# Kernel tuning notes

Measured on AMD Instinct MI355X. Metric: run time of the kernel, lower is better.

The kernel has to match this reference:

```python
import jax, jax.numpy as jnp
import numpy as np

B, S, D, H, F, E = 2, 1024, 1024, 16, 2048, 8
HD = D // H


def _ln(x, g, b, eps=1e-5):
    m = x.mean(-1, keepdims=True)
    v = ((x - m) ** 2).mean(-1, keepdims=True)
    return (x - m) / jnp.sqrt(v + eps) * g + b


def setup_inputs() -> dict:
    key = jax.random.key(0)
    ks = jax.random.split(key, 12)
    rn = lambda k, shp, s=0.02: jax.random.normal(k, shp, jnp.float32) * s
    return {
        'src': jax.random.normal(ks[0], (B, S, D), jnp.float32),
        'q_w': rn(ks[1], (D, D)),
        'k_w': rn(ks[2], (D, D)),
        'v_w': rn(ks[3], (D, D)),
        'out_w': rn(ks[4], (D, D)),
        'gate_w': rn(ks[5], (D, D)),
        'gate_b': rn(ks[6], (D,)),
        'scale_w': rn(ks[7], (H, HD)),
        'n1_g': jnp.ones((D,), jnp.float32),
        'n1_b': jnp.zeros((D,), jnp.float32),
        'n2_g': jnp.ones((D,), jnp.float32),
        'n2_b': jnp.zeros((D,), jnp.float32),
        'moe_gate_w': rn(ks[8], (D, E)),
        'moe_gate_b': jnp.zeros((E,), jnp.float32),
        'w1': rn(ks[9], (E, D, F)),
        'b1': jnp.zeros((E, F), jnp.float32),
        'ln_g': jnp.ones((E, F), jnp.float32),
        'ln_b': jnp.zeros((E, F), jnp.float32),
        'w2': rn(ks[10], (E, F, D)),
        'b2': jnp.zeros((E, D), jnp.float32),
        'res_scale': jnp.ones((E,), jnp.float32),
    }


def reference(src, q_w, k_w, v_w, out_w, gate_w, gate_b, scale_w,
              n1_g, n1_b, n2_g, n2_b, moe_gate_w, moe_gate_b,
              w1, b1, ln_g, ln_b, w2, b2, res_scale):
    b, s, d = src.shape
    h = scale_w.shape[0]
    hd = d // h
    # --- MemoAttention (gated, dynamically scaled), eval mode ---
    q = (src @ q_w).reshape(b, s, h, hd).transpose(0, 2, 1, 3)  # [b,h,s,hd]
    k = (src @ k_w).reshape(b, s, h, hd).transpose(0, 2, 1, 3)
    v = (src @ v_w).reshape(b, s, h, hd).transpose(0, 2, 1, 3)
    scores = jnp.einsum('bhqd,bhkd->bhqk', q, k) / np.float32(np.sqrt(hd))
    scale = jax.nn.sigmoid(jnp.einsum('bhsd,hd->bhs', q, scale_w)) * 2.0
    scores = scores * scale[..., None]
    aw = jax.nn.softmax(scores, axis=-1)
    out = jnp.einsum('bhqk,bhkd->bhqd', aw, v).transpose(0, 2, 1, 3).reshape(b, s, d)
    gate = jax.nn.sigmoid(out @ gate_w + gate_b)
    attn = (out * gate) @ out_w
    # --- residual + norm1 ---
    x = _ln(src + attn, n1_g, n1_b)
    # --- MoE FFN (top-2 routing; torch loop overwrites -> last (max-index) expert
    xr = x.reshape(-1, d)                      # [N, d]
    n = xr.shape[0]
    logits = xr @ moe_gate_w + moe_gate_b       # [N, E]
    top_v, top_i = jax.lax.top_k(logits, 2)
    wts = jax.nn.softmax(top_v, axis=-1)        # [N, 2]
    chosen = jnp.max(top_i, axis=-1)            # last-written expert per token

    def expert(W1, B1, G, Bt, W2, B2, rsc):
        hh = xr @ W1 + B1                       # [N, F]
        hh = jax.nn.gelu(_ln(hh, G, Bt), approximate=False)
        return (hh @ W2 + B2) * rsc + xr        # [N, d]

    outs = jax.vmap(expert)(w1, b1, ln_g, ln_b, w2, b2, res_scale)  # [E,N,d]
    sel = jnp.take_along_axis(outs.transpose(1, 0, 2), chosen[:, None, None], axis=1)[:, 0]
    moe = sel * jnp.sum(wts, axis=-1, keepdims=True)
    # --- residual + norm2 ---
    return _ln(x + moe.reshape(b, s, d), n2_g, n2_b)
```

## Files before the change

kernel.cpp:

```cpp
#include <hip/hip_runtime.h>


typedef _Float16 f16;
typedef _Float16 f16x8 __attribute__((ext_vector_type(8)));
typedef _Float16 f16x4 __attribute__((ext_vector_type(4)));
typedef float f32x4 __attribute__((ext_vector_type(4)));

constexpr int CS  = 1024;
constexpr int CD  = 1024;
constexpr int CH  = 16;
constexpr int CHD = 64;
constexpr int CF  = 2048;
constexpr int CE  = 8;
constexpr int CN  = 2048;
constexpr int CBH = 32;
constexpr int KS  = 512;
constexpr int MAXT = 24;

constexpr float LO_SCALE = 2048.f;
constexpr float LO_INV   = 1.f / 2048.f;

#define MFMA16(a, b, c) __builtin_amdgcn_mfma_f32_16x16x32_f16((a), (b), (c), 0, 0, 0)

#define TO_GBL(p) ((const __attribute__((address_space(1))) void*)(p))
#define TO_LDS(p) ((__attribute__((address_space(3))) void*)(p))
#define GLD16(g, l) __builtin_amdgcn_global_load_lds(TO_GBL(g), TO_LDS(l), 16, 0, 0)

__device__ __forceinline__ void fsplit(float v, f16 &hi, f16 &lo) {
  hi = (f16)v;
  lo = (f16)((v - (float)hi) * LO_SCALE);
}


__global__ void k_split_cvt(const float* __restrict__ in, f16* __restrict__ oh,
                            f16* __restrict__ ol, int n) {
  int i = (blockIdx.x * blockDim.x + threadIdx.x) * 4;
  if (i >= n) return;
  float4 v = *(const float4*)(in + i);
  float a[4] = {v.x, v.y, v.z, v.w};
  f16x4 vh, vl;
#pragma unroll
  for (int j = 0; j < 4; ++j) {
    f16 hi = (f16)a[j];
    vh[j] = hi;
    vl[j] = (f16)((a[j] - (float)hi) * LO_SCALE);
  }
  *(f16x4*)(oh + i) = vh;
  *(f16x4*)(ol + i) = vl;
}

__global__ __launch_bounds__(256) void k_transpose_split(
    const float* __restrict__ in, f16* __restrict__ oh,
    f16* __restrict__ ol, int R, int C) {
  __shared__ float t[64][65];
  const int z = blockIdx.z;
  const float* src = in + (size_t)z * R * C;
  f16* dh = oh + (size_t)z * R * C;
  f16* dl = ol ? ol + (size_t)z * R * C : nullptr;
  const int c0 = blockIdx.x * 64, r0 = blockIdx.y * 64;
  const int tt = threadIdx.x;
  const int lane = tt & 63, wv = tt >> 6;
#pragma unroll
  for (int i = 0; i < 16; ++i)
    t[wv + i * 4][lane] = src[(size_t)(r0 + wv + i * 4) * C + c0 + lane];
  __syncthreads();
  const int oc = tt >> 4;
  const int og = tt & 15;
#pragma unroll
  for (int cc = 0; cc < 64; cc += 16) {
    f16x4 vh, vl;
#pragma unroll
    for (int j = 0; j < 4; ++j) {
      const float v = t[og * 4 + j][cc + oc];
      f16 hi = (f16)v;
      vh[j] = hi;
      vl[j] = (f16)((v - (float)hi) * LO_SCALE);
    }
    const size_t idx = (size_t)(c0 + cc + oc) * R + r0 + og * 4;
    *(f16x4*)(dh + idx) = vh;
    if (dl) *(f16x4*)(dl + idx) = vl;
  }
}


template <bool SPLIT>
__device__ __forceinline__ void gemm_tile128(
    const f16* a0, const f16* a1, const f16* al0, const f16* al1,
    const f16* b0, const f16* b1, const f16* bl0, const f16* bl1,
    int K, f16* lds, f32x4 (&accm)[4][4], f32x4 (&accc)[4][4]) {
  constexpr int BUF = SPLIT ? 16384 : 8192;
  constexpr int BO  = SPLIT ? 8192 : 4096;
  const int t = threadIdx.x;
  const int lane = t & 63, wave = t >> 6;
  const int wm = wave >> 1, wn = wave & 1;
  const int m16 = lane & 15, quad = lane >> 4;
  int aoff[4], boff[4];
#pragma unroll
  for (int s = 0; s < 4; ++s) {
    const int ra = wm * 64 + s * 16 + m16;
    aoff[s] = ra * 32 + ((quad ^ ((ra >> 1) & 3)) * 8);
    const int rb = wn * 64 + s * 16 + m16;
    boff[s] = BO + rb * 32 + ((quad ^ ((rb >> 1) & 3)) * 8);
  }
  auto stage = [&](f16* buf) {
    GLD16(a0, buf + t * 8);
    GLD16(a1, buf + 2048 + t * 8);
    GLD16(b0, buf + BO + t * 8);
    GLD16(b1, buf + BO + 2048 + t * 8);
    if constexpr (SPLIT) {
      GLD16(al0, buf + 4096 + t * 8);
      GLD16(al1, buf + 6144 + t * 8);
      GLD16(bl0, buf + 12288 + t * 8);
      GLD16(bl1, buf + 14336 + t * 8);
      al0 += 32; al1 += 32; bl0 += 32; bl1 += 32;
    }
    a0 += 32; a1 += 32; b0 += 32; b1 += 32;
  };
  stage(lds);
  int cur = 0;
  for (int k = 0; k < K; k += 32) {
    __syncthreads();
    f16* buf = lds + cur * BUF;
    if (k + 32 < K) stage(lds + (cur ^ 1) * BUF);
    f16x8 af[4], alf[4];
#pragma unroll
    for (int s = 0; s < 4; ++s) {
      af[s] = *(const f16x8*)(buf + aoff[s]);
      if constexpr (SPLIT) alf[s] = *(const f16x8*)(buf + 4096 + aoff[s]);
    }
#pragma unroll
    for (int sn = 0; sn < 4; ++sn) {
      const f16x8 bf = *(const f16x8*)(buf + boff[sn]);
#pragma unroll
      for (int sm = 0; sm < 4; ++sm)
        accm[sm][sn] = MFMA16(af[sm], bf, accm[sm][sn]);
      if constexpr (SPLIT) {
        const f16x8 blf = *(const f16x8*)(buf + 4096 + boff[sn]);
#pragma unroll
        for (int sm = 0; sm < 4; ++sm)
          accc[sm][sn] = MFMA16(af[sm], blf, accc[sm][sn]);
#pragma unroll
        for (int sm = 0; sm < 4; ++sm)
          accc[sm][sn] = MFMA16(alf[sm], bf, accc[sm][sn]);
      }
    }
    cur ^= 1;
  }
}


__global__ __launch_bounds__(256, 2) void g_qkv(
    const f16* __restrict__ srcH, const f16* __restrict__ srcL,
    const f16* __restrict__ qwH, const f16* __restrict__ qwL,
    const f16* __restrict__ kwH, const f16* __restrict__ kwL,
    const f16* __restrict__ vwH, const f16* __restrict__ vwL,
    f16* __restrict__ qHo, f16* __restrict__ qLo,
    f16* __restrict__ kHo, f16* __restrict__ kLo,
    f16* __restrict__ vTH, f16* __restrict__ vTL) {
  __shared__ f16 lds[32768];
  const int z = blockIdx.z;
  const int m0 = blockIdx.x * 128, n0 = blockIdx.y * 128;
  const int t = threadIdx.x;
  const int rowS = t >> 2;
  const int ksw = ((t & 3) ^ ((rowS >> 1) & 3)) * 8;
  const f16* BH = (z == 0) ? qwH : (z == 1) ? kwH : vwH;
  const f16* BL = (z == 0) ? qwL : (z == 1) ? kwL : vwL;
  const f16* A0 = srcH + (size_t)(m0 + rowS) * CD + ksw;
  const f16* AL0 = srcL + (size_t)(m0 + rowS) * CD + ksw;
  const f16* B0 = BH + (size_t)(n0 + rowS) * CD + ksw;
  const f16* BL0 = BL + (size_t)(n0 + rowS) * CD + ksw;
  const f32x4 VZ = {0.f, 0.f, 0.f, 0.f};
  f32x4 accm[4][4], accc[4][4];
#pragma unroll
  for (int i = 0; i < 4; ++i)
#pragma unroll
    for (int j = 0; j < 4; ++j) { accm[i][j] = VZ; accc[i][j] = VZ; }
  gemm_tile128<true>(A0, A0 + (size_t)64 * CD, AL0, AL0 + (size_t)64 * CD,
                     B0, B0 + (size_t)64 * CD, BL0, BL0 + (size_t)64 * CD,
                     CD, lds, accm, accc);
  const int lane = t & 63, wave = t >> 6;
  const int wm = wave >> 1, wn = wave & 1;
  const int m16 = lane & 15, quad = lane >> 4;
#pragma unroll
  for (int sm = 0; sm < 4; ++sm)
#pragma unroll
    for (int sn = 0; sn < 4; ++sn)
#pragma unroll
      for (int r = 0; r < 4; ++r) {
        const int row = m0 + wm * 64 + sm * 16 + quad * 4 + r;
        const int col = n0 + wn * 64 + sn * 16 + m16;
        const float v = accm[sm][sn][r] + accc[sm][sn][r] * LO_INV;
        f16 hi, lo; fsplit(v, hi, lo);
        const int bb = row >> 10, ss = row & 1023;
        const int hh = col >> 6, hd = col & 63;
        if (z == 2) {
          const size_t idx = ((size_t)((bb * CH + hh) * CHD + hd)) * CS + ss;
          vTH[idx] = hi; vTL[idx] = lo;
        } else {
          const size_t idx = ((size_t)((bb * CH + hh) * CS + ss)) * CHD + hd;
          if (z == 0) { qHo[idx] = hi; qLo[idx] = lo; }
          else        { kHo[idx] = hi; kLo[idx] = lo; }
        }
      }
}


__device__ __forceinline__ int pswz(int q, int k) {
  return q * 64 + ((((k >> 2) ^ q) & 15) << 2) + (k & 3);
}

__global__ __launch_bounds__(256) void k_fattn(
    const f16* __restrict__ qH_, const f16* __restrict__ qL_,
    const f16* __restrict__ kH_, const f16* __restrict__ kL_,
    const f16* __restrict__ vTH_, const f16* __restrict__ vTL_,
    const float* __restrict__ scale_w,
    f16* __restrict__ aoH, f16* __restrict__ aoL) {
  __shared__ f16 kvb[32768];
  __shared__ float psc[4 * 1024];
  const int bh = blockIdx.y;
  const int b = bh >> 4, h = bh & 15;
  const int t = threadIdx.x;
  const int lane = t & 63, wave = t >> 6;
  const int m16 = lane & 15, quad = lane >> 4;
  const int q0 = blockIdx.x * 64 + wave * 16;
  float* P = psc + wave * 1024;
  const f32x4 VZ = {0.f, 0.f, 0.f, 0.f};
  const size_t kb = (size_t)bh * CS * CHD;

  const int rowS = t >> 3, chS = t & 7;
  auto stage = [&](f16* dst, int kc) {
#pragma unroll
    for (int i = 0; i < 2; ++i) {
      const int row = rowS + 32 * i;
      const int sc = (chS ^ (row & 7)) * 8;
      GLD16(kH_ + kb + (size_t)(kc + row) * CHD + sc, dst + i * 2048 + t * 8);
      GLD16(kL_ + kb + (size_t)(kc + row) * CHD + sc, dst + 4096 + i * 2048 + t * 8);
      GLD16(vTH_ + kb + (size_t)row * CS + kc + sc, dst + 8192 + i * 2048 + t * 8);
      GLD16(vTL_ + kb + (size_t)row * CS + kc + sc, dst + 12288 + i * 2048 + t * 8);
    }
  };
  auto ldf = [&](const f16* piece, int r, int q) -> f16x8 {
    return *(const f16x8*)(piece + r * 64 + ((q ^ (r & 7)) * 8));
  };

  const f16* qrh = qH_ + ((size_t)bh * CS + q0 + m16) * CHD + quad * 8;
  const f16* qrl = qL_ + ((size_t)bh * CS + q0 + m16) * CHD + quad * 8;
  f16x8 a0h = *(const f16x8*)(qrh);
  f16x8 a1h = *(const f16x8*)(qrh + 32);
  f16x8 a0l = *(const f16x8*)(qrl);
  f16x8 a1l = *(const f16x8*)(qrl + 32);

  stage(kvb, 0);

  float dot = 0.f;
  {
    const float* sw = scale_w + h * CHD + quad * 8;
    float4 s0 = *(const float4*)(sw);
    float4 s1 = *(const float4*)(sw + 4);
    float4 s2 = *(const float4*)(sw + 32);
    float4 s3 = *(const float4*)(sw + 36);
    float sv[16] = {s0.x, s0.y, s0.z, s0.w, s1.x, s1.y, s1.z, s1.w,
                    s2.x, s2.y, s2.z, s2.w, s3.x, s3.y, s3.z, s3.w};
#pragma unroll
    for (int j = 0; j < 8; ++j) {
      dot += ((float)a0h[j] + (float)a0l[j] * LO_INV) * sv[j];
      dot += ((float)a1h[j] + (float)a1l[j] * LO_INV) * sv[8 + j];
    }
    dot += __shfl_xor(dot, 16);
    dot += __shfl_xor(dot, 32);
  }
  const float qsv = 2.f / (1.f + __expf(-dot));
  float qsr[4];
#pragma unroll
  for (int r = 0; r < 4; ++r) qsr[r] = __shfl(qsv, quad * 4 + r) * 0.125f;

  f32x4 accm[4], accc[4], accd[4];
#pragma unroll
  for (int tt = 0; tt < 4; ++tt) { accm[tt] = VZ; accc[tt] = VZ; accd[tt] = VZ; }
  float mrun[4], lrun[4];
#pragma unroll
  for (int r = 0; r < 4; ++r) { mrun[r] = -1e30f; lrun[r] = 0.f; }

  int cur = 0;
  for (int kc = 0; kc < CS; kc += 64) {
    __syncthreads();
    const f16* kv = kvb + cur * 16384;
    if (kc + 64 < CS) stage(kvb + (cur ^ 1) * 16384, kc + 64);

    f32x4 st[4];
#pragma unroll
    for (int tt = 0; tt < 4; ++tt) {
      const int r = tt * 16 + m16;
      f16x8 b0h = ldf(kv,        r, quad);
      f16x8 b1h = ldf(kv,        r, quad + 4);
      f16x8 b0l = ldf(kv + 4096, r, quad);
      f16x8 b1l = ldf(kv + 4096, r, quad + 4);
      f32x4 am = VZ, ac1 = VZ, ac2 = VZ;
      am = MFMA16(a0h, b0h, am); am = MFMA16(a1h, b1h, am);
      ac1 = MFMA16(a0h, b0l, ac1); ac2 = MFMA16(a0l, b0h, ac2);
      ac1 = MFMA16(a1h, b1l, ac1); ac2 = MFMA16(a1l, b1h, ac2);
#pragma unroll
      for (int r4 = 0; r4 < 4; ++r4)
        st[tt][r4] = (am[r4] + (ac1[r4] + ac2[r4]) * LO_INV) * qsr[r4];
    }
    float alpha[4];
#pragma unroll
    for (int r = 0; r < 4; ++r) {
      float mx = fmaxf(fmaxf(st[0][r], st[1][r]), fmaxf(st[2][r], st[3][r]));
#pragma unroll
      for (int msk = 8; msk >= 1; msk >>= 1) mx = fmaxf(mx, __shfl_xor(mx, msk));
      const float mnew = fmaxf(mrun[r], mx);
      alpha[r] = __expf(mrun[r] - mnew);
      mrun[r] = mnew;
    }
    float rs[4] = {0.f, 0.f, 0.f, 0.f};
#pragma unroll
    for (int tt = 0; tt < 4; ++tt)
#pragma unroll
      for (int r = 0; r < 4; ++r) {
        const float e = __expf(st[tt][r] - mrun[r]);
        rs[r] += e;
        P[pswz(quad * 4 + r, tt * 16 + m16)] = e;
      }
#pragma unroll
    for (int r = 0; r < 4; ++r) {
#pragma unroll
      for (int msk = 8; msk >= 1; msk >>= 1) rs[r] += __shfl_xor(rs[r], msk);
      lrun[r] = lrun[r] * alpha[r] + rs[r];
#pragma unroll
      for (int tt = 0; tt < 4; ++tt) {
        accm[tt][r] *= alpha[r]; accc[tt][r] *= alpha[r]; accd[tt][r] *= alpha[r];
      }
    }
    f16x8 pah[2], pal[2];
#pragma unroll
    for (int c = 0; c < 2; ++c) {
      const int k0 = c * 32 + quad * 8;
      float4 p0 = *(const float4*)(P + pswz(m16, k0));
      float4 p1 = *(const float4*)(P + pswz(m16, k0 + 4));
      float pv[8] = {p0.x, p0.y, p0.z, p0.w, p1.x, p1.y, p1.z, p1.w};
#pragma unroll
      for (int j = 0; j < 8; ++j) {
        f16 hi = (f16)pv[j];
        pah[c][j] = hi;
        pal[c][j] = (f16)((pv[j] - (float)hi) * LO_SCALE);
      }
    }
#pragma unroll
    for (int c = 0; c < 2; ++c)
#pragma unroll
      for (int tt = 0; tt < 4; ++tt) {
        const int r = tt * 16 + m16;
        f16x8 vbh = ldf(kv + 8192,  r, quad + 4 * c);
        f16x8 vbl = ldf(kv + 12288, r, quad + 4 * c);
        accm[tt] = MFMA16(pah[c], vbh, accm[tt]);
        accc[tt] = MFMA16(pah[c], vbl, accc[tt]);
        accd[tt] = MFMA16(pal[c], vbh, accd[tt]);
      }
    cur ^= 1;
  }
#pragma unroll
  for (int tt = 0; tt < 4; ++tt)
#pragma unroll
    for (int r = 0; r < 4; ++r) {
      const int row = q0 + quad * 4 + r;
      const float v =
          (accm[tt][r] + (accc[tt][r] + accd[tt][r]) * LO_INV) / lrun[r];
      f16 hi, lo; fsplit(v, hi, lo);
      const size_t idx = ((size_t)(b * CS + row)) * CD + h * CHD + tt * 16 + m16;
      aoH[idx] = hi; aoL[idx] = lo;
    }
}


__global__ __launch_bounds__(256, 2) void g_gate(
    const f16* __restrict__ aoH, const f16* __restrict__ aoL,
    const f16* __restrict__ gwH, const f16* __restrict__ gwL,
    float* __restrict__ gpre ) {
  __shared__ f16 lds[32768];
  const int m0 = blockIdx.x * 128, n0 = blockIdx.y * 128, s = blockIdx.z;
  const int t = threadIdx.x;
  const int rowS = t >> 2;
  const int ksw = ((t & 3) ^ ((rowS >> 1) & 3)) * 8;
  const int k0 = s * KS;
  const f16* A0 = aoH + (size_t)(m0 + rowS) * CD + k0 + ksw;
  const f16* AL0 = aoL + (size_t)(m0 + rowS) * CD + k0 + ksw;
  const f16* B0 = gwH + (size_t)(n0 + rowS) * CD + k0 + ksw;
  const f16* BL0 = gwL + (size_t)(n0 + rowS) * CD + k0 + ksw;
  const f32x4 VZ = {0.f, 0.f, 0.f, 0.f};
  f32x4 accm[4][4], accc[4][4];
#pragma unroll
  for (int i = 0; i < 4; ++i)
#pragma unroll
    for (int j = 0; j < 4; ++j) { accm[i][j] = VZ; accc[i][j] = VZ; }
  gemm_tile128<true>(A0, A0 + (size_t)64 * CD, AL0, AL0 + (size_t)64 * CD,
                     B0, B0 + (size_t)64 * CD, BL0, BL0 + (size_t)64 * CD,
                     KS, lds, accm, accc);
  float* gp = gpre + (size_t)s * CN * CD;
  const int lane = t & 63, wave = t >> 6;
  const int wm = wave >> 1, wn = wave & 1;
  const int m16 = lane & 15, quad = lane >> 4;
#pragma unroll
  for (int sm = 0; sm < 4; ++sm)
#pragma unroll
    for (int sn = 0; sn < 4; ++sn)
#pragma unroll
      for (int r = 0; r < 4; ++r) {
        const int row = m0 + wm * 64 + sm * 16 + quad * 4 + r;
        const int col = n0 + wn * 64 + sn * 16 + m16;
        gp[(size_t)row * CD + col] = accm[sm][sn][r] + accc[sm][sn][r] * LO_INV;
      }
}

__global__ __launch_bounds__(256) void k_gatemul(
    const float* __restrict__ gpre, const f16* __restrict__ aoH,
    const f16* __restrict__ aoL, const float* __restrict__ gate_b,
    f16* __restrict__ gdH, f16* __restrict__ gdL) {
  const int i = (blockIdx.x * 256 + threadIdx.x) * 4;
  float4 p0 = *(const float4*)(gpre + i);
  float4 p1 = *(const float4*)(gpre + (size_t)CN * CD + i);
  float4 gb = *(const float4*)(gate_b + (i & (CD - 1)));
  f16x4 ah = *(const f16x4*)(aoH + i);
  f16x4 al = *(const f16x4*)(aoL + i);
  float pre[4] = {p0.x + p1.x + gb.x, p0.y + p1.y + gb.y,
                  p0.z + p1.z + gb.z, p0.w + p1.w + gb.w};
  f16x4 oh, ol;
#pragma unroll
  for (int j = 0; j < 4; ++j) {
    const float g = 1.f / (1.f + __expf(-pre[j]));
    const float ov = ((float)ah[j] + (float)al[j] * LO_INV) * g;
    f16 hi, lo; fsplit(ov, hi, lo);
    oh[j] = hi; ol[j] = lo;
  }
  *(f16x4*)(gdH + i) = oh;
  *(f16x4*)(gdL + i) = ol;
}

__global__ __launch_bounds__(256, 2) void g_outp(
    const f16* __restrict__ gdH, const f16* __restrict__ gdL,
    const f16* __restrict__ owH, const f16* __restrict__ owL,
    float* __restrict__ y1p ) {
  __shared__ f16 lds[32768];
  const int m0 = blockIdx.x * 128, n0 = blockIdx.y * 128, s = blockIdx.z;
  const int t = threadIdx.x;
  const int rowS = t >> 2;
  const int ksw = ((t & 3) ^ ((rowS >> 1) & 3)) * 8;
  const int k0 = s * KS;
  const f16* A0 = gdH + (size_t)(m0 + rowS) * CD + k0 + ksw;
  const f16* AL0 = gdL + (size_t)(m0 + rowS) * CD + k0 + ksw;
  const f16* B0 = owH + (size_t)(n0 + rowS) * CD + k0 + ksw;
  const f16* BL0 = owL + (size_t)(n0 + rowS) * CD + k0 + ksw;
  const f32x4 VZ = {0.f, 0.f, 0.f, 0.f};
  f32x4 accm[4][4], accc[4][4];
#pragma unroll
  for (int i = 0; i < 4; ++i)
#pragma unroll
    for (int j = 0; j < 4; ++j) { accm[i][j] = VZ; accc[i][j] = VZ; }
  gemm_tile128<true>(A0, A0 + (size_t)64 * CD, AL0, AL0 + (size_t)64 * CD,
                     B0, B0 + (size_t)64 * CD, BL0, BL0 + (size_t)64 * CD,
                     KS, lds, accm, accc);
  float* yp = y1p + (size_t)s * CN * CD;
  const int lane = t & 63, wave = t >> 6;
  const int wm = wave >> 1, wn = wave & 1;
  const int m16 = lane & 15, quad = lane >> 4;
#pragma unroll
  for (int sm = 0; sm < 4; ++sm)
#pragma unroll
    for (int sn = 0; sn < 4; ++sn)
#pragma unroll
      for (int r = 0; r < 4; ++r) {
        const int row = m0 + wm * 64 + sm * 16 + quad * 4 + r;
        const int col = n0 + wn * 64 + sn * 16 + m16;
        yp[(size_t)row * CD + col] = accm[sm][sn][r] + accc[sm][sn][r] * LO_INV;
      }
}


__device__ __forceinline__ void block_reduce2(float &s, float &ss, float* red) {
#pragma unroll
  for (int msk = 32; msk >= 1; msk >>= 1) {
    s += __shfl_xor(s, msk);
    ss += __shfl_xor(ss, msk);
  }
  const int wave = threadIdx.x >> 6, lane = threadIdx.x & 63;
  if (lane == 0) { red[wave] = s; red[4 + wave] = ss; }
  __syncthreads();
  s = red[0] + red[1] + red[2] + red[3];
  ss = red[4] + red[5] + red[6] + red[7];
}

__global__ __launch_bounds__(256) void k_ln1(
    const float* __restrict__ y1p, const float* __restrict__ srcp,
    const float* __restrict__ g, const float* __restrict__ bb,
    float* __restrict__ x, f16* __restrict__ xH) {
  __shared__ float red[8];
  const int n = blockIdx.x;
  const int t = threadIdx.x;
  const size_t off = (size_t)n * CD + t * 4;
  float4 v0 = *(const float4*)(y1p + off);
  float4 v1 = *(const float4*)(y1p + (size_t)CN * CD + off);
  float4 v2 = *(const float4*)(srcp + off);
  float a[4] = {v0.x + v1.x + v2.x, v0.y + v1.y + v2.y,
                v0.z + v1.z + v2.z, v0.w + v1.w + v2.w};
  float s = a[0] + a[1] + a[2] + a[3];
  float ss = a[0]*a[0] + a[1]*a[1] + a[2]*a[2] + a[3]*a[3];
  block_reduce2(s, ss, red);
  const float mean = s * (1.f / CD);
  const float var = ss * (1.f / CD) - mean * mean;
  const float rstd = rsqrtf(var + 1e-5f);
#pragma unroll
  for (int j = 0; j < 4; ++j) {
    const int d = t * 4 + j;
    const float val = (a[j] - mean) * rstd * g[d] + bb[d];
    x[(size_t)n * CD + d] = val;
    xH[(size_t)n * CD + d] = (f16)val;
  }
}

__global__ __launch_bounds__(256) void k_ln2(
    const float* __restrict__ zbp, const float* __restrict__ x,
    const float* __restrict__ b2, const float* __restrict__ rsc,
    const int* __restrict__ chosen,
    const float* __restrict__ g, const float* __restrict__ bb,
    float* __restrict__ outp) {
  __shared__ float red[8];
  const int n = blockIdx.x;
  const int e = chosen[n];
  const float rs = rsc[e];
  const int t = threadIdx.x;
  const size_t off = (size_t)n * CD + t * 4;
  float4 p0 = *(const float4*)(zbp + off);
  float4 p1 = *(const float4*)(zbp + (size_t)CN * CD + off);
  float4 p2 = *(const float4*)(zbp + (size_t)2 * CN * CD + off);
  float4 p3 = *(const float4*)(zbp + (size_t)3 * CN * CD + off);
  float4 xv = *(const float4*)(x + off);
  float4 bv = *(const float4*)(b2 + (size_t)e * CD + t * 4);
  float a[4] = {2.f * xv.x + (p0.x + p1.x + p2.x + p3.x + bv.x) * rs,
                2.f * xv.y + (p0.y + p1.y + p2.y + p3.y + bv.y) * rs,
                2.f * xv.z + (p0.z + p1.z + p2.z + p3.z + bv.z) * rs,
                2.f * xv.w + (p0.w + p1.w + p2.w + p3.w + bv.w) * rs};
  float s = a[0] + a[1] + a[2] + a[3];
  float ss = a[0]*a[0] + a[1]*a[1] + a[2]*a[2] + a[3]*a[3];
  block_reduce2(s, ss, red);
  const float mean = s * (1.f / CD);
  const float var = ss * (1.f / CD) - mean * mean;
  const float rstd = rsqrtf(var + 1e-5f);
#pragma unroll
  for (int j = 0; j < 4; ++j) {
    const int d = t * 4 + j;
    outp[(size_t)n * CD + d] = (a[j] - mean) * rstd * g[d] + bb[d];
  }
}


__global__ void k_zero_counts(int* counts) {
  if (threadIdx.x < CE) counts[threadIdx.x] = 0;
}

__global__ __launch_bounds__(256) void k_route(
    const float* __restrict__ x, const float* __restrict__ gw, const float* __restrict__ gb,
    int* __restrict__ chosen, int* __restrict__ counts, int* __restrict__ bucket) {
  const int wave = threadIdx.x >> 6, lane = threadIdx.x & 63;
  const int n = blockIdx.x * 4 + wave;
  const float* xr = x + (size_t)n * CD;
  float acc[CE];
#pragma unroll
  for (int e = 0; e < CE; ++e) acc[e] = 0.f;
  for (int j = 0; j < 16; ++j) {
    const int d = lane * 16 + j;
    const float xv = xr[d];
    const float* wr = gw + (size_t)d * CE;
#pragma unroll
    for (int e = 0; e < CE; ++e) acc[e] += xv * wr[e];
  }
#pragma unroll
  for (int msk = 32; msk >= 1; msk >>= 1) {
#pragma unroll
    for (int e = 0; e < CE; ++e) acc[e] += __shfl_xor(acc[e], msk);
  }
  if (lane == 0) {
    float best = -1e30f, second = -1e30f;
    int bi = 0, si = 0;
#pragma unroll
    for (int e = 0; e < CE; ++e) {
      const float L = acc[e] + gb[e];
      if (L > best) { second = best; si = bi; best = L; bi = e; }
      else if (L > second) { second = L; si = e; }
    }
    const int ch = bi > si ? bi : si;
    chosen[n] = ch;
    const int pos = atomicAdd(&counts[ch], 1);
    bucket[ch * CN + pos] = n;
  }
}

__global__ void k_plan(const int* __restrict__ counts, int* __restrict__ tiles) {
  if (threadIdx.x == 0) {
    int n = 0;
    for (int e = 0; e < CE; ++e) {
      const int c = counts[e];
      for (int m0 = 0; m0 < c; m0 += 128) { tiles[2 * n] = e; tiles[2 * n + 1] = m0; ++n; }
    }
    for (; n < MAXT; ++n) { tiles[2 * n] = -1; tiles[2 * n + 1] = 0; }
  }
}


__global__ __launch_bounds__(256, 2) void g_moe1(
    const f16* __restrict__ xH, const f16* __restrict__ w1t,
    const int* __restrict__ counts, const int* __restrict__ bucket,
    const int* __restrict__ tiles, float* __restrict__ hbp ) {
  const int e = tiles[2 * blockIdx.x];
  if (e < 0) return;
  const int m0 = tiles[2 * blockIdx.x + 1];
  const int cnt = counts[e];
  const int s = blockIdx.z;
  __shared__ f16 lds[16384];
  const int t = threadIdx.x;
  const int rowS = t >> 2;
  const int ksw = ((t & 3) ^ ((rowS >> 1) & 3)) * 8;
  const int k0 = s * KS;
  int ra0 = m0 + rowS;      if (ra0 > cnt - 1) ra0 = cnt - 1;
  int ra1 = m0 + rowS + 64; if (ra1 > cnt - 1) ra1 = cnt - 1;
  const int tok0 = bucket[e * CN + ra0];
  const int tok1 = bucket[e * CN + ra1];
  const int n0 = blockIdx.y * 128;
  const f16* B0 = w1t + ((size_t)e * CF + n0 + rowS) * CD + k0 + ksw;
  const f32x4 VZ = {0.f, 0.f, 0.f, 0.f};
  f32x4 accm[4][4], accd[4][4];
#pragma unroll
  for (int i = 0; i < 4; ++i)
#pragma unroll
    for (int j = 0; j < 4; ++j) { accm[i][j] = VZ; accd[i][j] = VZ; }
  gemm_tile128<false>(xH + (size_t)tok0 * CD + k0 + ksw,
                      xH + (size_t)tok1 * CD + k0 + ksw, nullptr, nullptr,
                      B0, B0 + (size_t)64 * CD, nullptr, nullptr,
                      KS, lds, accm, accd);
  float* hp = hbp + (size_t)s * CN * CF;
  const int lane = t & 63, wave = t >> 6;
  const int wm = wave >> 1, wn = wave & 1;
  const int m16 = lane & 15, quad = lane >> 4;
#pragma unroll
  for (int sm = 0; sm < 4; ++sm)
#pragma unroll
    for (int sn = 0; sn < 4; ++sn)
#pragma unroll
      for (int r = 0; r < 4; ++r) {
        const int rr = m0 + wm * 64 + sm * 16 + quad * 4 + r;
        if (rr >= cnt) continue;
        const int tok = bucket[e * CN + rr];
        const int col = n0 + wn * 64 + sn * 16 + m16;
        hp[(size_t)tok * CF + col] = accm[sm][sn][r];
      }
}

__global__ __launch_bounds__(256) void k_lngelu(
    const float* __restrict__ hbp, const int* __restrict__ chosen,
    const float* __restrict__ b1,
    const float* __restrict__ ln_g, const float* __restrict__ ln_b,
    f16* __restrict__ h2) {
  __shared__ float red[8];
  const int n = blockIdx.x;
  const int e = chosen[n];
  const int t = threadIdx.x;
  const size_t off = (size_t)n * CF + t * 8;
  float4 v0 = *(const float4*)(hbp + off);
  float4 v1 = *(const float4*)(hbp + off + 4);
  float4 u0 = *(const float4*)(hbp + (size_t)CN * CF + off);
  float4 u1 = *(const float4*)(hbp + (size_t)CN * CF + off + 4);
  float4 b0 = *(const float4*)(b1 + (size_t)e * CF + t * 8);
  float4 b1v = *(const float4*)(b1 + (size_t)e * CF + t * 8 + 4);
  float a[8] = {v0.x + u0.x + b0.x, v0.y + u0.y + b0.y,
                v0.z + u0.z + b0.z, v0.w + u0.w + b0.w,
                v1.x + u1.x + b1v.x, v1.y + u1.y + b1v.y,
                v1.z + u1.z + b1v.z, v1.w + u1.w + b1v.w};
  float s = 0.f, ss = 0.f;
#pragma unroll
  for (int j = 0; j < 8; ++j) { s += a[j]; ss += a[j] * a[j]; }
  block_reduce2(s, ss, red);
  const float mean = s * (1.f / CF);
  const float var = ss * (1.f / CF) - mean * mean;
  const float rstd = rsqrtf(var + 1e-5f);
  const float* g = ln_g + (size_t)e * CF;
  const float* bb = ln_b + (size_t)e * CF;
#pragma unroll
  for (int j = 0; j < 8; ++j) {
    const int d = t * 8 + j;
    const float val = (a[j] - mean) * rstd * g[d] + bb[d];
    const float gl = 0.5f * val * (1.f + erff(val * 0.70710678118654752f));
    h2[(size_t)n * CF + d] = (f16)gl;
  }
}

__global__ __launch_bounds__(256, 2) void g_moe2(
    const f16* __restrict__ h2, const f16* __restrict__ w2t,
    const int* __restrict__ counts, const int* __restrict__ bucket,
    const int* __restrict__ tiles, float* __restrict__ zbp ) {
  const int e = tiles[2 * blockIdx.x];
  if (e < 0) return;
  const int m0 = tiles[2 * blockIdx.x + 1];
  const int cnt = counts[e];
  const int s = blockIdx.z;
  __shared__ f16 lds[16384];
  const int t = threadIdx.x;
  const int rowS = t >> 2;
  const int ksw = ((t & 3) ^ ((rowS >> 1) & 3)) * 8;
  const int k0 = s * KS;
  int ra0 = m0 + rowS;      if (ra0 > cnt - 1) ra0 = cnt - 1;
  int ra1 = m0 + rowS + 64; if (ra1 > cnt - 1) ra1 = cnt - 1;
  const int tok0 = bucket[e * CN + ra0];
  const int tok1 = bucket[e * CN + ra1];
  const int n0 = blockIdx.y * 128;
  const f16* B0 = w2t + ((size_t)e * CD + n0 + rowS) * CF + k0 + ksw;
  const f32x4 VZ = {0.f, 0.f, 0.f, 0.f};
  f32x4 accm[4][4], accd[4][4];
#pragma unroll
  for (int i = 0; i < 4; ++i)
#pragma unroll
    for (int j = 0; j < 4; ++j) { accm[i][j] = VZ; accd[i][j] = VZ; }
  gemm_tile128<false>(h2 + (size_t)tok0 * CF + k0 + ksw,
                      h2 + (size_t)tok1 * CF + k0 + ksw, nullptr, nullptr,
                      B0, B0 + (size_t)64 * CF, nullptr, nullptr,
                      KS, lds, accm, accd);
  float* zp = zbp + (size_t)s * CN * CD;
  const int lane = t & 63, wave = t >> 6;
  const int wm = wave >> 1, wn = wave & 1;
  const int m16 = lane & 15, quad = lane >> 4;
#pragma unroll
  for (int sm = 0; sm < 4; ++sm)
#pragma unroll
    for (int sn = 0; sn < 4; ++sn)
#pragma unroll
      for (int r = 0; r < 4; ++r) {
        const int rr = m0 + wm * 64 + sm * 16 + quad * 4 + r;
        if (rr >= cnt) continue;
        const int tok = bucket[e * CN + rr];
        const int col = n0 + wn * 64 + sn * 16 + m16;
        zp[(size_t)tok * CD + col] = accm[sm][sn][r];
      }
}


extern "C" void kernel_launch(void* const* d_in, const int* in_sizes, int n_in,
                              void* d_out, int out_size, void* d_ws, size_t ws_size,
                              hipStream_t stream) {
  (void)in_sizes; (void)n_in; (void)out_size; (void)ws_size;
  const float* src        = (const float*)d_in[0];
  const float* q_w        = (const float*)d_in[1];
  const float* k_w        = (const float*)d_in[2];
  const float* v_w        = (const float*)d_in[3];
  const float* out_w      = (const float*)d_in[4];
  const float* gate_w     = (const float*)d_in[5];
  const float* gate_b     = (const float*)d_in[6];
  const float* scale_w    = (const float*)d_in[7];
  const float* n1_g       = (const float*)d_in[8];
  const float* n1_b       = (const float*)d_in[9];
  const float* n2_g       = (const float*)d_in[10];
  const float* n2_b       = (const float*)d_in[11];
  const float* moe_gate_w = (const float*)d_in[12];
  const float* moe_gate_b = (const float*)d_in[13];
  const float* w1         = (const float*)d_in[14];
  const float* b1         = (const float*)d_in[15];
  const float* ln_g       = (const float*)d_in[16];
  const float* ln_b       = (const float*)d_in[17];
  const float* w2         = (const float*)d_in[18];
  const float* b2         = (const float*)d_in[19];
  const float* res_scale  = (const float*)d_in[20];
  float* outp = (float*)d_out;

  char* p = (char*)d_ws;
  auto take = [&](size_t bytes) -> char* {
    char* r = p;
    p += (bytes + 255) & ~(size_t)255;
    return r;
  };
  f16* srcH = (f16*)take((size_t)CN * CD * 2);
  f16* srcL = (f16*)take((size_t)CN * CD * 2);
  f16* qwH = (f16*)take((size_t)CD * CD * 2);
  f16* qwL = (f16*)take((size_t)CD * CD * 2);
  f16* kwH = (f16*)take((size_t)CD * CD * 2);
  f16* kwL = (f16*)take((size_t)CD * CD * 2);
  f16* vwH = (f16*)take((size_t)CD * CD * 2);
  f16* vwL = (f16*)take((size_t)CD * CD * 2);
  f16* gwH = (f16*)take((size_t)CD * CD * 2);
  f16* gwL = (f16*)take((size_t)CD * CD * 2);
  f16* owH = (f16*)take((size_t)CD * CD * 2);
  f16* owL = (f16*)take((size_t)CD * CD * 2);
  f16* qH = (f16*)take((size_t)CBH * CS * CHD * 2);
  f16* qL = (f16*)take((size_t)CBH * CS * CHD * 2);
  f16* kH = (f16*)take((size_t)CBH * CS * CHD * 2);
  f16* kL = (f16*)take((size_t)CBH * CS * CHD * 2);
  f16* vTH = (f16*)take((size_t)CBH * CS * CHD * 2);
  f16* vTL = (f16*)take((size_t)CBH * CS * CHD * 2);
  f16* aoH = (f16*)take((size_t)CN * CD * 2);
  f16* aoL = (f16*)take((size_t)CN * CD * 2);
  f16* gdH = (f16*)take((size_t)CN * CD * 2);
  f16* gdL = (f16*)take((size_t)CN * CD * 2);
  float* x  = (float*)take((size_t)CN * CD * 4);
  f16* xH = (f16*)take((size_t)CN * CD * 2);
  int* counts = (int*)take(64);
  int* bucket = (int*)take((size_t)CE * CN * 4);
  int* chosen = (int*)take((size_t)CN * 4);
  int* tiles = (int*)take((size_t)MAXT * 2 * 4);
  f16* h2 = (f16*)take((size_t)CN * CF * 2);
  f16* w1t = (f16*)take((size_t)CE * CF * CD * 2);
  f16* w2t = (f16*)take((size_t)CE * CD * CF * 2);
  float* pbuf = (float*)take((size_t)4 * CN * CD * 4);

  k_split_cvt<<<dim3(CN * CD / 4 / 256), 256, 0, stream>>>(src, srcH, srcL, CN * CD);
  k_transpose_split<<<dim3(CD / 64, CD / 64, 1), 256, 0, stream>>>(q_w, qwH, qwL, CD, CD);
  k_transpose_split<<<dim3(CD / 64, CD / 64, 1), 256, 0, stream>>>(k_w, kwH, kwL, CD, CD);
  k_transpose_split<<<dim3(CD / 64, CD / 64, 1), 256, 0, stream>>>(v_w, vwH, vwL, CD, CD);
  k_transpose_split<<<dim3(CD / 64, CD / 64, 1), 256, 0, stream>>>(gate_w, gwH, gwL, CD, CD);
  k_transpose_split<<<dim3(CD / 64, CD / 64, 1), 256, 0, stream>>>(out_w, owH, owL, CD, CD);
  k_transpose_split<<<dim3(CF / 64, CD / 64, CE), 256, 0, stream>>>(w1, w1t, nullptr, CD, CF);
  k_transpose_split<<<dim3(CD / 64, CF / 64, CE), 256, 0, stream>>>(w2, w2t, nullptr, CF, CD);

  g_qkv<<<dim3(CN / 128, CD / 128, 3), 256, 0, stream>>>(
      srcH, srcL, qwH, qwL, kwH, kwL, vwH, vwL, qH, qL, kH, kL, vTH, vTL);
  k_fattn<<<dim3(CS / 64, CBH), 256, 0, stream>>>(
      qH, qL, kH, kL, vTH, vTL, scale_w, aoH, aoL);
  g_gate<<<dim3(CN / 128, CD / 128, 2), 256, 0, stream>>>(aoH, aoL, gwH, gwL, pbuf);
  k_gatemul<<<dim3(CN * CD / 4 / 256), 256, 0, stream>>>(pbuf, aoH, aoL, gate_b, gdH, gdL);
  g_outp<<<dim3(CN / 128, CD / 128, 2), 256, 0, stream>>>(gdH, gdL, owH, owL, pbuf);
  k_ln1<<<dim3(CN), 256, 0, stream>>>(pbuf, src, n1_g, n1_b, x, xH);

  k_zero_counts<<<dim3(1), 64, 0, stream>>>(counts);
  k_route<<<dim3(CN / 4), 256, 0, stream>>>(x, moe_gate_w, moe_gate_b, chosen, counts, bucket);
  k_plan<<<dim3(1), 64, 0, stream>>>(counts, tiles);
  g_moe1<<<dim3(MAXT, CF / 128, 2), 256, 0, stream>>>(xH, w1t, counts, bucket, tiles, pbuf);
  k_lngelu<<<dim3(CN), 256, 0, stream>>>(pbuf, chosen, b1, ln_g, ln_b, h2);
  g_moe2<<<dim3(MAXT, CD / 128, 4), 256, 0, stream>>>(h2, w2t, counts, bucket, tiles, pbuf);
  k_ln2<<<dim3(CN), 256, 0, stream>>>(pbuf, x, b2, res_scale, chosen, n2_g, n2_b, outp);
}
```

Baseline: 515.5 us.

## Process two query tiles per attention block with lazy rescale and exp2 softmax

```diff
diff --git a/kernel.cpp b/kernel.cpp
--- a/kernel.cpp
+++ b/kernel.cpp
@@ -181,27 +181,44 @@
   const int lane = t & 63, wave = t >> 6;
   const int wm = wave >> 1, wn = wave & 1;
   const int m16 = lane & 15, quad = lane >> 4;
-#pragma unroll
-  for (int sm = 0; sm < 4; ++sm)
-#pragma unroll
-    for (int sn = 0; sn < 4; ++sn)
-#pragma unroll
-      for (int r = 0; r < 4; ++r) {
-        const int row = m0 + wm * 64 + sm * 16 + quad * 4 + r;
+  if (z == 2) {
+#pragma unroll
+    for (int sm = 0; sm < 4; ++sm)
+#pragma unroll
+      for (int sn = 0; sn < 4; ++sn) {
+        const int row0 = m0 + wm * 64 + sm * 16 + quad * 4;
         const int col = n0 + wn * 64 + sn * 16 + m16;
-        const float v = accm[sm][sn][r] + accc[sm][sn][r] * LO_INV;
-        f16 hi, lo; fsplit(v, hi, lo);
-        const int bb = row >> 10, ss = row & 1023;
+        f16x4 vh, vl;
+#pragma unroll
+        for (int r = 0; r < 4; ++r) {
+          const float v = accm[sm][sn][r] + accc[sm][sn][r] * LO_INV;
+          f16 hi, lo; fsplit(v, hi, lo);
+          vh[r] = hi; vl[r] = lo;
+        }
+        const int bb = row0 >> 10, ss = row0 & 1023;
         const int hh = col >> 6, hd = col & 63;
-        if (z == 2) {
-          const size_t idx = ((size_t)((bb * CH + hh) * CHD + hd)) * CS + ss;
-          vTH[idx] = hi; vTL[idx] = lo;
-        } else {
+        const size_t idx = ((size_t)((bb * CH + hh) * CHD + hd)) * CS + ss;
+        *(f16x4*)(vTH + idx) = vh;
+        *(f16x4*)(vTL + idx) = vl;
+      }
+  } else {
+#pragma unroll
+    for (int sm = 0; sm < 4; ++sm)
+#pragma unroll
+      for (int sn = 0; sn < 4; ++sn)
+#pragma unroll
+        for (int r = 0; r < 4; ++r) {
+          const int row = m0 + wm * 64 + sm * 16 + quad * 4 + r;
+          const int col = n0 + wn * 64 + sn * 16 + m16;
+          const float v = accm[sm][sn][r] + accc[sm][sn][r] * LO_INV;
+          f16 hi, lo; fsplit(v, hi, lo);
+          const int bb = row >> 10, ss = row & 1023;
+          const int hh = col >> 6, hd = col & 63;
           const size_t idx = ((size_t)((bb * CH + hh) * CS + ss)) * CHD + hd;
           if (z == 0) { qHo[idx] = hi; qLo[idx] = lo; }
           else        { kHo[idx] = hi; kLo[idx] = lo; }
         }
-      }
+  }
 }
 
 
@@ -217,12 +234,13 @@
     f16* __restrict__ aoH, f16* __restrict__ aoL) {
   __shared__ f16 kvb[32768];
   __shared__ float psc[4 * 1024];
-  const int bh = blockIdx.y;
+  const int id = blockIdx.x + 8 * blockIdx.y;
+  const int w = (id & 7) * 32 + (id >> 3);
+  const int bh = w >> 3, qc = w & 7;
   const int b = bh >> 4, h = bh & 15;
   const int t = threadIdx.x;
   const int lane = t & 63, wave = t >> 6;
   const int m16 = lane & 15, quad = lane >> 4;
-  const int q0 = blockIdx.x * 64 + wave * 16;
   float* P = psc + wave * 1024;
   const f32x4 VZ = {0.f, 0.f, 0.f, 0.f};
   const size_t kb = (size_t)bh * CS * CHD;
@@ -243,16 +261,21 @@
     return *(const f16x8*)(piece + r * 64 + ((q ^ (r & 7)) * 8));
   };
 
-  const f16* qrh = qH_ + ((size_t)bh * CS + q0 + m16) * CHD + quad * 8;
-  const f16* qrl = qL_ + ((size_t)bh * CS + q0 + m16) * CHD + quad * 8;
-  f16x8 a0h = *(const f16x8*)(qrh);
-  f16x8 a1h = *(const f16x8*)(qrh + 32);
-  f16x8 a0l = *(const f16x8*)(qrl);
-  f16x8 a1l = *(const f16x8*)(qrl + 32);
+  f16x8 a0h[2], a1h[2], a0l[2], a1l[2];
+#pragma unroll
+  for (int qi = 0; qi < 2; ++qi) {
+    const int qbase = qc * 128 + qi * 64 + wave * 16;
+    const f16* qrh = qH_ + ((size_t)bh * CS + qbase + m16) * CHD + quad * 8;
+    const f16* qrl = qL_ + ((size_t)bh * CS + qbase + m16) * CHD + quad * 8;
+    a0h[qi] = *(const f16x8*)(qrh);
+    a1h[qi] = *(const f16x8*)(qrh + 32);
+    a0l[qi] = *(const f16x8*)(qrl);
+    a1l[qi] = *(const f16x8*)(qrl + 32);
+  }
 
   stage(kvb, 0);
 
-  float dot = 0.f;
+  float qsl[2][4];
   {
     const float* sw = scale_w + h * CHD + quad * 8;
     float4 s0 = *(const float4*)(sw);
@@ -262,24 +285,31 @@
     float sv[16] = {s0.x, s0.y, s0.z, s0.w, s1.x, s1.y, s1.z, s1.w,
                     s2.x, s2.y, s2.z, s2.w, s3.x, s3.y, s3.z, s3.w};
 #pragma unroll
-    for (int j = 0; j < 8; ++j) {
-      dot += ((float)a0h[j] + (float)a0l[j] * LO_INV) * sv[j];
-      dot += ((float)a1h[j] + (float)a1l[j] * LO_INV) * sv[8 + j];
-    }
-    dot += __shfl_xor(dot, 16);
-    dot += __shfl_xor(dot, 32);
-  }
-  const float qsv = 2.f / (1.f + __expf(-dot));
-  float qsr[4];
-#pragma unroll
-  for (int r = 0; r < 4; ++r) qsr[r] = __shfl(qsv, quad * 4 + r) * 0.125f;
-
-  f32x4 accm[4], accc[4], accd[4];
-#pragma unroll
-  for (int tt = 0; tt < 4; ++tt) { accm[tt] = VZ; accc[tt] = VZ; accd[tt] = VZ; }
-  float mrun[4], lrun[4];
-#pragma unroll
-  for (int r = 0; r < 4; ++r) { mrun[r] = -1e30f; lrun[r] = 0.f; }
+    for (int qi = 0; qi < 2; ++qi) {
+      float dot = 0.f;
+#pragma unroll
+      for (int j = 0; j < 8; ++j) {
+        dot += ((float)a0h[qi][j] + (float)a0l[qi][j] * LO_INV) * sv[j];
+        dot += ((float)a1h[qi][j] + (float)a1l[qi][j] * LO_INV) * sv[8 + j];
+      }
+      dot += __shfl_xor(dot, 16);
+      dot += __shfl_xor(dot, 32);
+      const float qsv = 2.f / (1.f + __expf(-dot)) * (0.125f * 1.44269504f);
+#pragma unroll
+      for (int r = 0; r < 4; ++r) qsl[qi][r] = __shfl(qsv, quad * 4 + r);
+    }
+  }
+
+  f32x4 accm[2][4], accc[2][4];
+#pragma unroll
+  for (int qi = 0; qi < 2; ++qi)
+#pragma unroll
+    for (int tt = 0; tt < 4; ++tt) { accm[qi][tt] = VZ; accc[qi][tt] = VZ; }
+  float mrun[2][4], lrun[2][4];
+#pragma unroll
+  for (int qi = 0; qi < 2; ++qi)
+#pragma unroll
+    for (int r = 0; r < 4; ++r) { mrun[qi][r] = -1e30f; lrun[qi][r] = 0.f; }
 
   int cur = 0;
   for (int kc = 0; kc < CS; kc += 64) {
@@ -287,7 +317,7 @@
     const f16* kv = kvb + cur * 16384;
     if (kc + 64 < CS) stage(kvb + (cur ^ 1) * 16384, kc + 64);
 
-    f32x4 st[4];
+    f32x4 st[2][4];
 #pragma unroll
     for (int tt = 0; tt < 4; ++tt) {
       const int r = tt * 16 + m16;
@@ -295,81 +325,105 @@
       f16x8 b1h = ldf(kv,        r, quad + 4);
       f16x8 b0l = ldf(kv + 4096, r, quad);
       f16x8 b1l = ldf(kv + 4096, r, quad + 4);
-      f32x4 am = VZ, ac1 = VZ, ac2 = VZ;
-      am = MFMA16(a0h, b0h, am); am = MFMA16(a1h, b1h, am);
-      ac1 = MFMA16(a0h, b0l, ac1); ac2 = MFMA16(a0l, b0h, ac2);
-      ac1 = MFMA16(a1h, b1l, ac1); ac2 = MFMA16(a1l, b1h, ac2);
-#pragma unroll
-      for (int r4 = 0; r4 < 4; ++r4)
-        st[tt][r4] = (am[r4] + (ac1[r4] + ac2[r4]) * LO_INV) * qsr[r4];
-    }
-    float alpha[4];
-#pragma unroll
-    for (int r = 0; r < 4; ++r) {
-      float mx = fmaxf(fmaxf(st[0][r], st[1][r]), fmaxf(st[2][r], st[3][r]));
-#pragma unroll
-      for (int msk = 8; msk >= 1; msk >>= 1) mx = fmaxf(mx, __shfl_xor(mx, msk));
-      const float mnew = fmaxf(mrun[r], mx);
-      alpha[r] = __expf(mrun[r] - mnew);
-      mrun[r] = mnew;
-    }
-    float rs[4] = {0.f, 0.f, 0.f, 0.f};
+#pragma unroll
+      for (int qi = 0; qi < 2; ++qi) {
+        f32x4 am = VZ, ac1 = VZ, ac2 = VZ;
+        am = MFMA16(a0h[qi], b0h, am); am = MFMA16(a1h[qi], b1h, am);
+        ac1 = MFMA16(a0h[qi], b0l, ac1); ac2 = MFMA16(a0l[qi], b0h, ac2);
+        ac1 = MFMA16(a1h[qi], b1l, ac1); ac2 = MFMA16(a1l[qi], b1h, ac2);
+#pragma unroll
+        for (int r4 = 0; r4 < 4; ++r4)
+          st[qi][tt][r4] = (am[r4] + (ac1[r4] + ac2[r4]) * LO_INV) * qsl[qi][r4];
+      }
+    }
+#pragma unroll
+    for (int qi = 0; qi < 2; ++qi) {
+      float mx[4];
+      bool grow = false;
+#pragma unroll
+      for (int r = 0; r < 4; ++r) {
+        float m = fmaxf(fmaxf(st[qi][0][r], st[qi][1][r]),
+                        fmaxf(st[qi][2][r], st[qi][3][r]));
+#pragma unroll
+        for (int msk = 8; msk >= 1; msk >>= 1) m = fmaxf(m, __shfl_xor(m, msk));
+        mx[r] = m;
+        grow = grow || (m > mrun[qi][r]);
+      }
+      if (__any(grow)) {
+#pragma unroll
+        for (int r = 0; r < 4; ++r) {
+          const float mnew = fmaxf(mrun[qi][r], mx[r]);
+          const float alpha = exp2f(mrun[qi][r] - mnew);
+          mrun[qi][r] = mnew;
+          lrun[qi][r] *= alpha;
+#pragma unroll
+          for (int tt = 0; tt < 4; ++tt) {
+            accm[qi][tt][r] *= alpha;
+            accc[qi][tt][r] *= alpha;
+          }
+        }
+      }
+      float rs[4] = {0.f, 0.f, 0.f, 0.f};
+#pragma unroll
+      for (int tt = 0; tt < 4; ++tt)
+#pragma unroll
+        for (int r = 0; r < 4; ++r) {
+          const float e = exp2f(st[qi][tt][r] - mrun[qi][r]);
+          rs[r] += e;
+          P[pswz(quad * 4 + r, tt * 16 + m16)] = e;
+        }
+#pragma unroll
+      for (int r = 0; r < 4; ++r) {
+#pragma unroll
+        for (int msk = 8; msk >= 1; msk >>= 1) rs[r] += __shfl_xor(rs[r], msk);
+        lrun[qi][r] += rs[r];
+      }
+      f16x8 pah[2], pal[2];
+#pragma unroll
+      for (int c = 0; c < 2; ++c) {
+        const int k0 = c * 32 + quad * 8;
+        float4 p0 = *(const float4*)(P + pswz(m16, k0));
+        float4 p1 = *(const float4*)(P + pswz(m16, k0 + 4));
+        float pv[8] = {p0.x, p0.y, p0.z, p0.w, p1.x, p1.y, p1.z, p1.w};
+#pragma unroll
+        for (int j = 0; j < 8; ++j) {
+          f16 hi = (f16)pv[j];
+          pah[c][j] = hi;
+          pal[c][j] = (f16)((pv[j] - (float)hi) * LO_SCALE);
+        }
+      }
+#pragma unroll
+      for (int c = 0; c < 2; ++c) {
+        f16x8 vbh[4];
+#pragma unroll
+        for (int tt = 0; tt < 4; ++tt) {
+          const int r = tt * 16 + m16;
+          vbh[tt] = ldf(kv + 8192, r, quad + 4 * c);
+          f16x8 vbl = ldf(kv + 12288, r, quad + 4 * c);
+          accm[qi][tt] = MFMA16(pah[c], vbh[tt], accm[qi][tt]);
+          accc[qi][tt] = MFMA16(pah[c], vbl, accc[qi][tt]);
+        }
+#pragma unroll
+        for (int tt = 0; tt < 4; ++tt)
+          accc[qi][tt] = MFMA16(pal[c], vbh[tt], accc[qi][tt]);
+      }
+    }
+    cur ^= 1;
+  }
+#pragma unroll
+  for (int qi = 0; qi < 2; ++qi)
 #pragma unroll
     for (int tt = 0; tt < 4; ++tt)
 #pragma unroll
       for (int r = 0; r < 4; ++r) {
-        const float e = __expf(st[tt][r] - mrun[r]);
-        rs[r] += e;
-        P[pswz(quad * 4 + r, tt * 16 + m16)] = e;
-      }
-#pragma unroll
-    for (int r = 0; r < 4; ++r) {
-#pragma unroll
-      for (int msk = 8; msk >= 1; msk >>= 1) rs[r] += __shfl_xor(rs[r], msk);
-      lrun[r] = lrun[r] * alpha[r] + rs[r];
-#pragma unroll
-      for (int tt = 0; tt < 4; ++tt) {
-        accm[tt][r] *= alpha[r]; accc[tt][r] *= alpha[r]; accd[tt][r] *= alpha[r];
-      }
-    }
-    f16x8 pah[2], pal[2];
-#pragma unroll
-    for (int c = 0; c < 2; ++c) {
-      const int k0 = c * 32 + quad * 8;
-      float4 p0 = *(const float4*)(P + pswz(m16, k0));
-      float4 p1 = *(const float4*)(P + pswz(m16, k0 + 4));
-      float pv[8] = {p0.x, p0.y, p0.z, p0.w, p1.x, p1.y, p1.z, p1.w};
-#pragma unroll
-      for (int j = 0; j < 8; ++j) {
-        f16 hi = (f16)pv[j];
-        pah[c][j] = hi;
-        pal[c][j] = (f16)((pv[j] - (float)hi) * LO_SCALE);
-      }
-    }
-#pragma unroll
-    for (int c = 0; c < 2; ++c)
-#pragma unroll
-      for (int tt = 0; tt < 4; ++tt) {
-        const int r = tt * 16 + m16;
-        f16x8 vbh = ldf(kv + 8192,  r, quad + 4 * c);
-        f16x8 vbl = ldf(kv + 12288, r, quad + 4 * c);
-        accm[tt] = MFMA16(pah[c], vbh, accm[tt]);
-        accc[tt] = MFMA16(pah[c], vbl, accc[tt]);
-        accd[tt] = MFMA16(pal[c], vbh, accd[tt]);
-      }
-    cur ^= 1;
-  }
-#pragma unroll
-  for (int tt = 0; tt < 4; ++tt)
-#pragma unroll
-    for (int r = 0; r < 4; ++r) {
-      const int row = q0 + quad * 4 + r;
-      const float v =
-          (accm[tt][r] + (accc[tt][r] + accd[tt][r]) * LO_INV) / lrun[r];
-      f16 hi, lo; fsplit(v, hi, lo);
-      const size_t idx = ((size_t)(b * CS + row)) * CD + h * CHD + tt * 16 + m16;
-      aoH[idx] = hi; aoL[idx] = lo;
-    }
+        const int row = qc * 128 + qi * 64 + wave * 16 + quad * 4 + r;
+        const float v =
+            (accm[qi][tt][r] + accc[qi][tt][r] * LO_INV) / lrun[qi][r];
+        f16 hi, lo; fsplit(v, hi, lo);
+        const size_t idx =
+            ((size_t)(b * CS + row)) * CD + h * CHD + tt * 16 + m16;
+        aoH[idx] = hi; aoL[idx] = lo;
+      }
 }
 
 
@@ -818,7 +872,7 @@
 
   g_qkv<<<dim3(CN / 128, CD / 128, 3), 256, 0, stream>>>(
       srcH, srcL, qwH, qwL, kwH, kwL, vwH, vwL, qH, qL, kH, kL, vTH, vTL);
-  k_fattn<<<dim3(CS / 64, CBH), 256, 0, stream>>>(
+  k_fattn<<<dim3(CS / 128, CBH), 256, 0, stream>>>(
       qH, qL, kH, kL, vTH, vTL, scale_w, aoH, aoL);
   g_gate<<<dim3(CN / 128, CD / 128, 2), 256, 0, stream>>>(aoH, aoL, gwH, gwL, pbuf);
   k_gatemul<<<dim3(CN * CD / 4 / 256), 256, 0, stream>>>(pbuf, aoH, aoL, gate_b, gdH, gdL);
```

Result: slower. 533.4 us (+3.5%).
